# Performance work log

Hardware: AMD Instinct MI355X
Metric: run time of the kernel (lower is better)

## Reference

```python
import jax, jax.numpy as jnp
import numpy as np

N_E = 512; KEY_DIM = 512; E_DIM = 512; E_SPLIT = 8
KT = 0.1; COE_EMA = 0.5; RATE = 1.2
HALF_PI = float(np.pi / 2.0)


def l2n(x, eps=1e-12):
    # torch F.normalize(p=2, dim=-1)
    return x / jnp.maximum(jnp.linalg.norm(x, axis=-1, keepdims=True), eps)


def sphere_emb(feature, t):
    # TimeSphereEncoder: lift unit feature in R^d to R^{d+1} with time angle
    # a = t * (pi/2) / rate ; out = [feature*cos(a), sin(a)]
    a = t * (HALF_PI / RATE)
    return jnp.concatenate([feature * jnp.cos(a)[..., None], jnp.sin(a)[..., None]], axis=-1)


def split_t_f(x):
    # inverse of sphere_emb for unit-norm x: recover (t, sin_component, feature)
    s = x[..., -1]
    t = jnp.arcsin(jnp.clip(s, -1.0, 1.0)) / (HALF_PI / RATE)
    f = l2n(x[..., :-1])
    return t, s, f


def split_norm(v):
    # split_vparams_norm: L2-normalize each of E_SPLIT contiguous chunks
    shp = v.shape
    d = E_DIM // E_SPLIT
    return l2n(v.reshape(shp[:-1] + (E_SPLIT, d))).reshape(shp)


def setup_inputs() -> dict:
    key = jax.random.key(0)
    k = jax.random.split(key, 6)
    key_soft = jax.random.normal(k[0], (32, 1024, KEY_DIM), jnp.float32)
    u_t = jax.random.uniform(k[1], (32, 1024), jnp.float32)
    keys_weight = l2n(jax.random.uniform(k[2], (N_E, KEY_DIM), jnp.float32, -1.0 / N_E, 1.0 / N_E))
    t_keys_weight = (jnp.arange(N_E, dtype=jnp.float32)[:, None]
                     + jax.random.uniform(k[3], (N_E, 1), jnp.float32)) / N_E
    r_keys_weight = jnp.full((N_E, 1), 0.999, jnp.float32)
    vparams_weight = jax.random.uniform(k[4], (N_E, E_DIM), jnp.float32, -1.0 / N_E, 1.0 / N_E)
    return {"key_soft": key_soft, "u_t": u_t, "keys_weight": keys_weight,
            "t_keys_weight": t_keys_weight, "r_keys_weight": r_keys_weight,
            "vparams_weight": vparams_weight}


def _forward(key_soft, u_t, keys_weight, t_keys_weight, r_keys_weight, vparams_weight):
    sg = jax.lax.stop_gradient
    B, T, D = key_soft.shape
    BT = B * T
    # normalize + time-embed tokens
    ks_emb = sphere_emb(l2n(key_soft), u_t)                       # (B,T,D+1)
    ks_flat = ks_emb.reshape(BT, D + 1)
    # codebook keys: normalized, time-embedded, detached, scaled by hardtanh(r)
    keys_norm = sphere_emb(l2n(keys_weight), t_keys_weight[:, 0])  # (n_e,D+1)
    r = jnp.clip(r_keys_weight, 0.0, 1.0)                          # (n_e,1)
    keysA = sg(keys_norm) * r
    score0 = ks_flat @ keysA.T                                     # (BT,n_e)
    idx0 = jnp.argmax(score0, axis=1)
    # --- EMA codebook update (all no-grad) ---
    ks_sg = sg(ks_flat)
    seg = jax.ops.segment_sum(ks_sg, idx0, num_segments=N_E)       # (n_e,D+1)
    cnt = jax.ops.segment_sum(jnp.ones((BT,), ks_sg.dtype), idx0, num_segments=N_E)[:, None]
    mean_ks = jnp.nan_to_num(seg / (1.0 + cnt))
    keys_new_full = l2n(sg(keysA) * COE_EMA + mean_ks * (1.0 - COE_EMA))
    t_new, _, feat_new = split_t_f(keys_new_full)
    index_switch = jnp.argsort(t_new)
    t_sorted = t_new[index_switch]
    keys_feat2 = feat_new[index_switch]
    r2 = jnp.clip(r_keys_weight[index_switch], 0.0, 1.0)
    vparams2 = vparams_weight[index_switch]
    idx1 = index_switch[idx0]
    cnt2 = jax.ops.segment_sum(jnp.ones((BT,), ks_sg.dtype), idx1, num_segments=N_E) + 1.0
    w_cnt = sg(jnp.nan_to_num(1.0 / cnt2)[idx1].reshape(B, T))
    # --- second scoring with updated codebook ---
    keys_norm2 = sphere_emb(l2n(keys_feat2), t_sorted)             # (n_e,D+1)
    keysB = sg(keys_norm2) * r2
    score = ks_flat @ keysB.T                                      # (BT,n_e)
    w = jnp.nan_to_num(jax.nn.softmax(score / KT, axis=-1))
    w_max = jnp.take_along_axis(w, idx1[:, None], axis=-1)[:, 0].reshape(B, T)
    vpn = split_norm(vparams2)
    vp_w = split_norm(w @ sg(vpn))                                 # (BT,e_dim)
    key_w = l2n(w @ sg(keysB))                                     # (BT,D+1)
    vparams_hard = split_norm(vparams2[idx1])
    key_hard_raw = keysB[idx1]
    vparams_hard = vp_w + sg(vparams_hard - vp_w)                  # straight-through
    key_hard = key_w + sg(key_hard_raw - key_w)
    return (idx1.reshape(B, T),
            key_hard.reshape(B, T, D + 1),
            vp_w.reshape(B, T, E_DIM),
            vparams_hard.reshape(B, T, E_DIM),
            w_max, w_cnt, ks_emb)


def reference(key_soft, u_t, keys_weight, t_keys_weight, r_keys_weight, vparams_weight):
    return _forward(key_soft, u_t, keys_weight, t_keys_weight, r_keys_weight, vparams_weight)
```

## Files before the change

kernel.cpp:

```cpp
#include <hip/hip_runtime.h>
#include <math.h>

constexpr int BT  = 32768;
constexpr int D   = 512;
constexpr int D1  = 513;
constexpr int NE  = 512;
constexpr int EDIM = 512;
constexpr int NCH = 128;
constexpr int SUB = 16;
constexpr int P1S = 520;
constexpr int AKP = 544;
#define KA 1.3089969389957472f

typedef _Float16 h16;
typedef _Float16 f16x8 __attribute__((ext_vector_type(8)));
typedef _Float16 f16x4 __attribute__((ext_vector_type(4)));
typedef _Float16 f16x2 __attribute__((ext_vector_type(2)));
typedef float f32x4 __attribute__((ext_vector_type(4)));

__device__ __forceinline__ float wave_sum(float v) {
#pragma unroll
  for (int off = 32; off; off >>= 1) v += __shfl_xor(v, off);
  return v;
}

__global__ __launch_bounds__(256) void k_embed(const float* __restrict__ ks,
                                               const float* __restrict__ ut,
                                               float* __restrict__ emb) {
  int token = blockIdx.x * 4 + (threadIdx.x >> 6);
  int lane = threadIdx.x & 63;
  const float* row = ks + (size_t)token * D;
  float v[8]; float ss = 0.f;
#pragma unroll
  for (int i = 0; i < 8; i++) { v[i] = row[lane + 64 * i]; ss += v[i] * v[i]; }
  ss = wave_sum(ss);
  float inv = 1.0f / fmaxf(sqrtf(ss), 1e-12f);
  float a = ut[token] * KA;
  float c = cosf(a), s = sinf(a);
  float* o = emb + (size_t)token * D1;
#pragma unroll
  for (int i = 0; i < 8; i++) o[lane + 64 * i] = v[i] * inv * c;
  if (lane == 0) o[D] = s;
}

__global__ __launch_bounds__(64) void k_keysA(const float* __restrict__ kw,
                                              const float* __restrict__ tk,
                                              const float* __restrict__ rk,
                                              float* __restrict__ keysA) {
  int e = blockIdx.x; int lane = threadIdx.x;
  const float* row = kw + (size_t)e * D;
  float v[8]; float ss = 0.f;
#pragma unroll
  for (int i = 0; i < 8; i++) { v[i] = row[lane + 64 * i]; ss += v[i] * v[i]; }
  ss = wave_sum(ss);
  float inv = 1.0f / fmaxf(sqrtf(ss), 1e-12f);
  float a = tk[e] * KA;
  float r = fminf(fmaxf(rk[e], 0.f), 1.f);
  float c = cosf(a) * r, s = sinf(a) * r;
  float* o = keysA + (size_t)e * D1;
#pragma unroll
  for (int i = 0; i < 8; i++) o[lane + 64 * i] = v[i] * inv * c;
  if (lane == 0) o[D] = s;
}

__global__ __launch_bounds__(64) void k_split2(const float* __restrict__ in,
                                               h16* __restrict__ out,
                                               int ncol, int kp) {
  int e = blockIdx.x; int lane = threadIdx.x;
  const float* r = in + (size_t)e * ncol;
  h16* o = out + (size_t)e * 2 * kp;
  for (int c = lane; c < kp; c += 64) {
    float x = (c < ncol) ? r[c] * 8.0f : 0.f;
    h16 h = (h16)x;
    o[c] = h;
    o[kp + c] = (h16)(x - (float)h);
  }
}

template <int KP, int EPI, int ASRC>
__global__ __launch_bounds__(256) void k_gemm3(const float* __restrict__ Af,
                                               const h16* __restrict__ Ai,
                                               const h16* __restrict__ Bp,
                                               float* __restrict__ C,
                                               unsigned int* __restrict__ W,
                                               float* __restrict__ pv,
                                               int* __restrict__ pi_,
                                               float* __restrict__ ps) {
  constexpr int NS = KP / 32;
  constexpr int LST = 36;
  __shared__ h16 Ah[128 * LST];
  __shared__ h16 Al[128 * LST];
  __shared__ h16 Bh[128 * LST];
  __shared__ h16 Bl[128 * LST];
  const int tid = threadIdx.x;
  const int bid = blockIdx.x;
  const int wg = (bid & 7) * (gridDim.x >> 3) + (bid >> 3);
  const int m0 = (wg >> 2) * 128;
  const int n0 = (wg & 3) * 128;
  const int nblk = wg & 3;
  const int lane = tid & 63;
  const int wid = tid >> 6;
  const int wr = wid >> 1, wc = wid & 1;
  const int l15 = lane & 15, l4 = lane >> 4;
  const int aB = (wr * 64 + l15) * LST + l4 * 8;
  const int bB = (wc * 64 + l15) * LST + l4 * 8;

  f32x4 acc[4][4] = {};

  auto loadAf = [&](int s, float fv[4][4]) {
    int k0 = s * 32;
    bool guard = (KP == AKP) && (k0 + 32 > D1);
#pragma unroll
    for (int p = 0; p < 4; ++p) {
      int row = (tid >> 3) + 32 * p;
      int fq = tid & 7;
      const float* ap = Af + (size_t)(m0 + row) * D1 + k0 + fq * 4;
      if (!guard) {
#pragma unroll
        for (int j = 0; j < 4; ++j) fv[p][j] = ap[j];
      } else {
#pragma unroll
        for (int j = 0; j < 4; ++j) {
          int c = k0 + fq * 4 + j;
          fv[p][j] = (c < D1) ? ap[j] : 0.f;
        }
      }
    }
  };
  auto writeAf = [&](float fv[4][4]) {
#pragma unroll
    for (int p = 0; p < 4; ++p) {
      int row = (tid >> 3) + 32 * p;
      int fq = tid & 7;
      f16x4 hh, ll;
#pragma unroll
      for (int j = 0; j < 4; ++j) {
        float x = fv[p][j] * 8.0f;
        h16 h = (h16)x;
        hh[j] = h;
        ll[j] = (h16)(x - (float)h);
      }
      *(f16x4*)&Ah[row * LST + fq * 4] = hh;
      *(f16x4*)&Al[row * LST + fq * 4] = ll;
    }
  };
  auto loadAi = [&](int s, uint4 av[4]) {
    int k0 = s * 32;
#pragma unroll
    for (int p = 0; p < 4; ++p) {
      int lin = tid + 256 * p;
      int row = lin >> 3, q = lin & 7;
      av[p] = *(const uint4*)(Ai + (size_t)(m0 + row) * (2 * KP) + k0 * 2 + q * 8);
    }
  };
  auto writeAi = [&](uint4 av[4]) {
#pragma unroll
    for (int p = 0; p < 4; ++p) {
      int lin = tid + 256 * p;
      int row = lin >> 3, q = lin & 7;
      f16x8 r = *(f16x8*)&av[p];
      f16x4 hh = {r[0], r[2], r[4], r[6]};
      f16x4 ll = {r[1], r[3], r[5], r[7]};
      *(f16x4*)&Ah[row * LST + q * 4] = hh;
      *(f16x4*)&Al[row * LST + q * 4] = ll;
    }
  };
  auto loadB = [&](int s, uint4 bv[4]) {
    int k0 = s * 32;
#pragma unroll
    for (int p = 0; p < 4; ++p) {
      int lin = tid + 256 * p;
      int row = (lin >> 2) & 127;
      int half = lin >> 9;
      int q = lin & 3;
      bv[p] = *(const uint4*)(Bp + (size_t)(n0 + row) * (2 * KP) + half * KP + k0 + q * 8);
    }
  };
  auto writeB = [&](uint4 bv[4]) {
#pragma unroll
    for (int p = 0; p < 4; ++p) {
      int lin = tid + 256 * p;
      int row = (lin >> 2) & 127;
      int half = lin >> 9;
      int q = lin & 3;
      h16* dst = half ? Bl : Bh;
      *(uint4*)&dst[row * LST + q * 8] = bv[p];
    }
  };

  {
    uint4 bv[4];
    loadB(0, bv);
    if constexpr (ASRC == 0) { float fv[4][4]; loadAf(0, fv); writeAf(fv); }
    else { uint4 av[4]; loadAi(0, av); writeAi(av); }
    writeB(bv);
  }
  __syncthreads();

  for (int s = 0; s < NS; ++s) {
    uint4 avn[4], bvn[4]; float fvn[4][4];
    if (s + 1 < NS) {
      if constexpr (ASRC == 0) loadAf(s + 1, fvn);
      else loadAi(s + 1, avn);
      loadB(s + 1, bvn);
    }
    f16x8 ah[4], al_[4];
#pragma unroll
    for (int i = 0; i < 4; ++i) {
      ah[i] = *(const f16x8*)&Ah[aB + i * 16 * LST];
      al_[i] = *(const f16x8*)&Al[aB + i * 16 * LST];
    }
#pragma unroll
    for (int j = 0; j < 4; ++j) {
      f16x8 bh_ = *(const f16x8*)&Bh[bB + j * 16 * LST];
      f16x8 bl_ = *(const f16x8*)&Bl[bB + j * 16 * LST];
#pragma unroll
      for (int i = 0; i < 4; ++i) {
        acc[i][j] = __builtin_amdgcn_mfma_f32_16x16x32_f16(ah[i], bh_, acc[i][j], 0, 0, 0);
        acc[i][j] = __builtin_amdgcn_mfma_f32_16x16x32_f16(al_[i], bh_, acc[i][j], 0, 0, 0);
        acc[i][j] = __builtin_amdgcn_mfma_f32_16x16x32_f16(ah[i], bl_, acc[i][j], 0, 0, 0);
      }
    }
    __syncthreads();
    if (s + 1 < NS) {
      if constexpr (ASRC == 0) writeAf(fvn);
      else writeAi(avn);
      writeB(bvn);
    }
    __syncthreads();
  }

  if constexpr (EPI == 1) {
#pragma unroll
    for (int i = 0; i < 4; ++i)
#pragma unroll
      for (int r = 0; r < 4; ++r) {
        float ss = 0.f;
#pragma unroll
        for (int j = 0; j < 4; ++j) ss += acc[i][j][r] * acc[i][j][r];
        ss += __shfl_xor(ss, 1); ss += __shfl_xor(ss, 2);
        ss += __shfl_xor(ss, 4); ss += __shfl_xor(ss, 8);
        float inv = 1.0f / fmaxf(sqrtf(ss), 1e-12f);
        int row = m0 + wr * 64 + i * 16 + l4 * 4 + r;
        float* cp = C + (size_t)row * 512 + n0 + wc * 64 + l15;
#pragma unroll
        for (int j = 0; j < 4; ++j) cp[j * 16] = acc[i][j][r] * inv;
      }
  } else if constexpr (EPI == 2) {
    float* lv = (float*)Ah;
    int*   li = (int*)Bh;
#pragma unroll
    for (int i = 0; i < 4; ++i)
#pragma unroll
      for (int r = 0; r < 4; ++r) {
        float bv = -INFINITY; int bidx = 0x7fffffff;
#pragma unroll
        for (int j = 0; j < 4; ++j) {
          float val = acc[i][j][r] * 0.015625f;
          int col = n0 + wc * 64 + j * 16 + l15;
          if (val > bv || (val == bv && col < bidx)) { bv = val; bidx = col; }
        }
#pragma unroll
        for (int off = 1; off < 16; off <<= 1) {
          float ov = __shfl_xor(bv, off);
          int oi = __shfl_xor(bidx, off);
          if (ov > bv || (ov == bv && oi < bidx)) { bv = ov; bidx = oi; }
        }
        if (l15 == 0) {
          int lr = wr * 64 + i * 16 + l4 * 4 + r;
          lv[wc * 128 + lr] = bv; li[wc * 128 + lr] = bidx;
        }
      }
    __syncthreads();
    if (tid < 128) {
      float v0 = lv[tid], v1 = lv[128 + tid];
      int i0 = li[tid], i1 = li[128 + tid];
      bool sec = (v1 > v0) || (v1 == v0 && i1 < i0);
      int row = m0 + tid;
      pv[(size_t)row * 4 + nblk] = sec ? v1 : v0;
      pi_[(size_t)row * 4 + nblk] = sec ? i1 : i0;
    }
  } else if constexpr (EPI == 3) {
    float* psW = (float*)Bh;
#pragma unroll
    for (int i = 0; i < 4; ++i)
#pragma unroll
      for (int r = 0; r < 4; ++r) {
        int row = m0 + wr * 64 + i * 16 + l4 * 4 + r;
        unsigned int* wp = W + (size_t)row * 512 + n0 + wc * 64 + l15;
        float se = 0.f;
#pragma unroll
        for (int j = 0; j < 4; ++j) {
          float v = acc[i][j][r] * 0.015625f;
          float w = __expf(10.f * v);
          se += w;
          h16 hh = (h16)w;
          f16x2 pk = {hh, (h16)(w - (float)hh)};
          wp[j * 16] = *(unsigned int*)&pk;
        }
        se += __shfl_xor(se, 1); se += __shfl_xor(se, 2);
        se += __shfl_xor(se, 4); se += __shfl_xor(se, 8);
        if (l15 == 0) psW[wc * 128 + wr * 64 + i * 16 + l4 * 4 + r] = se;
      }
    __syncthreads();
    if (tid < 128)
      ps[(size_t)(m0 + tid) * 4 + nblk] = psW[tid] + psW[128 + tid];
  }
}

__global__ __launch_bounds__(256) void k_argmax_fin(const float* __restrict__ pval,
                                                    const int* __restrict__ pidx,
                                                    int* __restrict__ idx0) {
  int t = blockIdx.x * 256 + threadIdx.x;
  float bv = pval[(size_t)t * 4];
  int bi = pidx[(size_t)t * 4];
#pragma unroll
  for (int b = 1; b < 4; ++b) {
    float v = pval[(size_t)t * 4 + b];
    if (v > bv) { bv = v; bi = pidx[(size_t)t * 4 + b]; }
  }
  idx0[t] = bi;
}

__global__ __launch_bounds__(256) void k_smfin(const float* __restrict__ ps,
                                               const unsigned int* __restrict__ W,
                                               const int* __restrict__ idx1,
                                               float* __restrict__ O4) {
  int t = blockIdx.x * 256 + threadIdx.x;
  float S = ps[(size_t)t * 4] + ps[(size_t)t * 4 + 1]
          + ps[(size_t)t * 4 + 2] + ps[(size_t)t * 4 + 3];
  unsigned int u = W[(size_t)t * 512 + idx1[t]];
  f16x2 pk = *(f16x2*)&u;
  float wsel = (float)pk[0] + (float)pk[1];
  O4[t] = wsel / S;
}

__global__ __launch_bounds__(256) void k_hist_chunks(const int* __restrict__ idx0,
                                                     int* __restrict__ hist2,
                                                     int* __restrict__ myrank) {
  __shared__ int lidx[256];
  __shared__ int hist[NE];
  int tid = threadIdx.x;
  int chunk = blockIdx.x;
  int t = chunk * 256 + tid;
  lidx[tid] = idx0[t];
  hist[tid] = 0; hist[tid + 256] = 0;
  __syncthreads();
  int j = lidx[tid];
  int rank = 0;
  for (int i = 0; i < tid; ++i) rank += (lidx[i] == j);
  myrank[t] = rank;
  atomicAdd(&hist[j], 1);
  __syncthreads();
  hist2[chunk * NE + tid] = hist[tid];
  hist2[chunk * NE + tid + 256] = hist[tid + 256];
}

__global__ __launch_bounds__(512) void k_scan(const int* __restrict__ hist2,
                                              int* __restrict__ offs,
                                              int* __restrict__ chunk_base,
                                              float* __restrict__ cntf) {
  __shared__ int sh[NE];
  int c = threadIdx.x;
  int tot = 0;
  for (int k = 0; k < NCH; ++k) tot += hist2[k * NE + c];
  cntf[c] = (float)tot;
  sh[c] = tot;
  __syncthreads();
  for (int off = 1; off < NE; off <<= 1) {
    int v = (c >= off) ? sh[c - off] : 0;
    __syncthreads();
    sh[c] += v;
    __syncthreads();
  }
  int excl = sh[c] - tot;
  offs[c] = excl;
  int run = excl;
  for (int k = 0; k < NCH; ++k) {
    chunk_base[k * NE + c] = run;
    run += hist2[k * NE + c];
  }
}

__global__ __launch_bounds__(256) void k_scatter(const int* __restrict__ idx0,
                                                 const int* __restrict__ myrank,
                                                 const int* __restrict__ chunk_base,
                                                 int* __restrict__ tok_sorted) {
  int tid = threadIdx.x;
  int chunk = blockIdx.x;
  int t = chunk * 256 + tid;
  int j = idx0[t];
  tok_sorted[chunk_base[chunk * NE + j] + myrank[t]] = t;
}

__global__ __launch_bounds__(256) void k_seg1(const int* __restrict__ tok_sorted,
                                              const int* __restrict__ offs,
                                              const float* __restrict__ cntf,
                                              const float* __restrict__ emb,
                                              float* __restrict__ part1) {
  __shared__ float part[4][512];
  __shared__ float p512[4];
  int e = blockIdx.x, sub = blockIdx.y;
  int tid = threadIdx.x;
  int wave = tid >> 6, lane = tid & 63;
  int start = offs[e];
  int n = (int)cntf[e];
  float acc[8] = {}; float a512 = 0.f;
  for (int k = sub * 4 + wave; k < n; k += SUB * 4) {
    int t = tok_sorted[start + k];
    const float* row = emb + (size_t)t * D1;
#pragma unroll
    for (int i = 0; i < 8; ++i) acc[i] += row[lane + 64 * i];
    if (lane == 0) a512 += row[512];
  }
#pragma unroll
  for (int i = 0; i < 8; ++i) part[wave][lane + 64 * i] = acc[i];
  if (lane == 0) p512[wave] = a512;
  __syncthreads();
  float* o = part1 + (size_t)(e * SUB + sub) * P1S;
  o[tid] = part[0][tid] + part[1][tid] + part[2][tid] + part[3][tid];
  o[tid + 256] = part[0][tid + 256] + part[1][tid + 256] + part[2][tid + 256] + part[3][tid + 256];
  if (tid == 0) o[512] = p512[0] + p512[1] + p512[2] + p512[3];
}

__global__ __launch_bounds__(256) void k_seg2(const float* __restrict__ part1,
                                              const float* __restrict__ cntf,
                                              const float* __restrict__ keysA,
                                              float* __restrict__ feat,
                                              float* __restrict__ tnew) {
  __shared__ float r4[4];
  __shared__ float r4b[4];
  int e = blockIdx.x;
  int tid = threadIdx.x;
  int wave = tid >> 6, lane = tid & 63;
  float s0 = 0.f, s1 = 0.f, s512 = 0.f;
  for (int sub = 0; sub < SUB; ++sub) {
    const float* p = part1 + (size_t)(e * SUB + sub) * P1S;
    s0 += p[tid]; s1 += p[tid + 256]; s512 += p[512];
  }
  float c = cntf[e];
  float rinv = 1.0f / (1.0f + c);
  float x0 = keysA[(size_t)e * D1 + tid] * 0.5f + (s0 * rinv) * 0.5f;
  float x1 = keysA[(size_t)e * D1 + tid + 256] * 0.5f + (s1 * rinv) * 0.5f;
  float x512 = keysA[(size_t)e * D1 + 512] * 0.5f + (s512 * rinv) * 0.5f;
  float ssp = x0 * x0 + x1 * x1;
  float w = wave_sum(ssp);
  if (lane == 0) r4[wave] = w;
  __syncthreads();
  float ss = r4[0] + r4[1] + r4[2] + r4[3] + x512 * x512;
  float inv = 1.0f / fmaxf(sqrtf(ss), 1e-12f);
  if (tid == 0) {
    float sc = fminf(fmaxf(x512 * inv, -1.0f), 1.0f);
    tnew[e] = asinf(sc) / KA;
  }
  float f0 = x0 * inv, f1 = x1 * inv;
  float ssp2 = f0 * f0 + f1 * f1;
  float w2 = wave_sum(ssp2);
  if (lane == 0) r4b[wave] = w2;
  __syncthreads();
  float ss2 = r4b[0] + r4b[1] + r4b[2] + r4b[3];
  float inv2 = 1.0f / fmaxf(sqrtf(ss2), 1e-12f);
  feat[(size_t)e * D + tid] = f0 * inv2;
  feat[(size_t)e * D + tid + 256] = f1 * inv2;
}

__global__ __launch_bounds__(512) void k_argsort(const float* __restrict__ tnew,
                                                 int* __restrict__ perm) {
  __shared__ float t[NE];
  int i = threadIdx.x;
  t[i] = tnew[i];
  __syncthreads();
  float ti = t[i];
  int rank = 0;
  for (int j = 0; j < NE; j++) {
    float tj = t[j];
    rank += (tj < ti) || (tj == ti && j < i);
  }
  perm[rank] = i;
}

__global__ __launch_bounds__(64) void k_build(const int* __restrict__ perm,
                                              const float* __restrict__ tnew,
                                              const float* __restrict__ rk,
                                              const float* __restrict__ feat,
                                              const float* __restrict__ vparams,
                                              float* __restrict__ keysB,
                                              float* __restrict__ vpn,
                                              h16* __restrict__ BV) {
  int p = blockIdx.x; int lane = threadIdx.x;
  int src = perm[p];
  float t = tnew[src];
  float a = t * KA;
  float r2 = fminf(fmaxf(rk[src], 0.f), 1.f);
  float f[8]; float ss = 0.f;
#pragma unroll
  for (int i = 0; i < 8; i++) { f[i] = feat[(size_t)src * D + lane + 64 * i]; ss += f[i] * f[i]; }
  ss = wave_sum(ss);
  float inv = 1.0f / fmaxf(sqrtf(ss), 1e-12f);
  float c = cosf(a) * r2, s = sinf(a) * r2;
#pragma unroll
  for (int i = 0; i < 8; i++) keysB[(size_t)p * D1 + lane + 64 * i] = f[i] * inv * c;
  if (lane == 0) keysB[(size_t)p * D1 + D] = s;
#pragma unroll
  for (int i = 0; i < 8; i++) {
    float vp = vparams[(size_t)src * EDIM + lane + 64 * i];
    float ssc = wave_sum(vp * vp);
    float invc = 1.0f / fmaxf(sqrtf(ssc), 1e-12f);
    float val = vp * invc;
    int d = lane + 64 * i;
    vpn[(size_t)p * EDIM + d] = val;
    float x = val * 8.0f;
    h16 hi = (h16)x;
    BV[(size_t)d * (2 * NE) + p] = hi;
    BV[(size_t)d * (2 * NE) + NE + p] = (h16)(x - (float)hi);
  }
}

__global__ __launch_bounds__(256) void k_idx1(const int* __restrict__ idx0,
                                              const int* __restrict__ perm,
                                              int* __restrict__ idx1,
                                              float* __restrict__ O0) {
  int t = blockIdx.x * 256 + threadIdx.x;
  int j = perm[idx0[t]];
  idx1[t] = j;
  O0[t] = (float)j;
}

__global__ __launch_bounds__(256) void k_gather(const int* __restrict__ idx1,
                                                const int* __restrict__ perm,
                                                const float* __restrict__ cntf,
                                                const float* __restrict__ keysB,
                                                const float* __restrict__ vpn,
                                                float* __restrict__ O1,
                                                float* __restrict__ O3,
                                                float* __restrict__ O5) {
  int t = blockIdx.x * 4 + (threadIdx.x >> 6);
  int lane = threadIdx.x & 63;
  int j = idx1[t];
#pragma unroll
  for (int i = 0; i < 9; i++) {
    int d = lane + 64 * i;
    if (d < D1) O1[(size_t)t * D1 + d] = keysB[(size_t)j * D1 + d];
  }
#pragma unroll
  for (int i = 0; i < 8; i++) {
    int d = lane + 64 * i;
    O3[(size_t)t * EDIM + d] = vpn[(size_t)j * EDIM + d];
  }
  if (lane == 0) O5[t] = 1.0f / (cntf[perm[j]] + 1.0f);
}

extern "C" void kernel_launch(void* const* d_in, const int* in_sizes, int n_in,
                              void* d_out, int out_size, void* d_ws, size_t ws_size,
                              hipStream_t stream) {
  const float* key_soft = (const float*)d_in[0];
  const float* u_t      = (const float*)d_in[1];
  const float* keys_w   = (const float*)d_in[2];
  const float* t_keys   = (const float*)d_in[3];
  const float* r_keys   = (const float*)d_in[4];
  const float* vparams  = (const float*)d_in[5];

  float* out = (float*)d_out;
  float* O0 = out;
  float* O1 = O0 + (size_t)BT;
  float* O2 = O1 + (size_t)BT * D1;
  float* O3 = O2 + (size_t)BT * EDIM;
  float* O4 = O3 + (size_t)BT * EDIM;
  float* O5 = O4 + (size_t)BT;
  float* O6 = O5 + (size_t)BT;

  float* ws = (float*)d_ws;
  size_t off = 0;
  auto alloc = [&](size_t n) { float* p = ws + off; off += (n + 63) & ~(size_t)63; return p; };
  unsigned int* w16 = (unsigned int*)alloc((size_t)BT * 512);
  float* part1  = alloc((size_t)NE * SUB * P1S);
  float* keysA  = alloc((size_t)NE * D1);
  float* keysB  = alloc((size_t)NE * D1);
  float* feat   = alloc((size_t)NE * D);
  float* vpn    = alloc((size_t)NE * EDIM);
  float* tnew   = alloc(NE);
  float* cntf   = alloc(NE);
  h16*   BA     = (h16*)alloc((size_t)NE * AKP);
  h16*   BB     = (h16*)alloc((size_t)NE * AKP);
  h16*   BV     = (h16*)alloc((size_t)EDIM * NE);
  float* pval   = alloc((size_t)BT * 4);
  int*   pidx   = (int*)alloc((size_t)BT * 4);
  float* ps2    = alloc((size_t)BT * 4);
  int*   idx0   = (int*)alloc(BT);
  int*   idx1   = (int*)alloc(BT);
  int*   perm   = (int*)alloc(NE);
  int*   myrank = (int*)alloc(BT);
  int*   tok_sorted = (int*)alloc(BT);
  int*   hist2  = (int*)alloc((size_t)NCH * NE);
  int*   chunk_base = (int*)alloc((size_t)NCH * NE);
  int*   offsb  = (int*)alloc(NE);

  k_embed<<<BT / 4, 256, 0, stream>>>(key_soft, u_t, O6);
  k_keysA<<<NE, 64, 0, stream>>>(keys_w, t_keys, r_keys, keysA);
  k_split2<<<NE, 64, 0, stream>>>(keysA, BA, D1, AKP);
  k_gemm3<AKP, 2, 0><<<1024, 256, 0, stream>>>(O6, nullptr, BA,
                                               nullptr, nullptr, pval, pidx, nullptr);
  k_argmax_fin<<<BT / 256, 256, 0, stream>>>(pval, pidx, idx0);
  k_hist_chunks<<<NCH, 256, 0, stream>>>(idx0, hist2, myrank);
  k_scan<<<1, NE, 0, stream>>>(hist2, offsb, chunk_base, cntf);
  k_scatter<<<NCH, 256, 0, stream>>>(idx0, myrank, chunk_base, tok_sorted);
  k_seg1<<<dim3(NE, SUB), 256, 0, stream>>>(tok_sorted, offsb, cntf, O6, part1);
  k_seg2<<<NE, 256, 0, stream>>>(part1, cntf, keysA, feat, tnew);
  k_argsort<<<1, NE, 0, stream>>>(tnew, perm);
  k_build<<<NE, 64, 0, stream>>>(perm, tnew, r_keys, feat, vparams, keysB, vpn, BV);
  k_split2<<<NE, 64, 0, stream>>>(keysB, BB, D1, AKP);
  k_idx1<<<BT / 256, 256, 0, stream>>>(idx0, perm, idx1, O0);
  k_gemm3<AKP, 3, 0><<<1024, 256, 0, stream>>>(O6, nullptr, BB,
                                               nullptr, w16, nullptr, nullptr, ps2);
  k_smfin<<<BT / 256, 256, 0, stream>>>(ps2, w16, idx1, O4);
  k_gemm3<512, 1, 1><<<1024, 256, 0, stream>>>(nullptr, (const h16*)w16, BV,
                                               O2, nullptr, nullptr, nullptr, nullptr);
  k_gather<<<BT / 4, 256, 0, stream>>>(idx1, perm, cntf, keysB, vpn, O1, O3, O5);
}
```

Before: 505.4 us.

## Cut split-fp16 GEMM terms per stage and store softmax weights as single fp16

Adds a TERMS template parameter so each GEMM runs only as many split-precision MFMA products as it needs. The first scoring GEMM keeps three terms because argmax needs accuracy. The second scoring GEMM drops the B-low term, and the weighted-value GEMM uses a single fp16 term. The softmax weight buffer shrinks from packed hi/lo fp16 pairs to one fp16 per element, halving its write and read traffic. The embed kernel is also changed to vectorized float4 loads. The price is lower precision in w and vp_w, which risks tolerance failures.

```diff
diff --git a/kernel.cpp b/kernel.cpp
--- a/kernel.cpp
+++ b/kernel.cpp
@@ -15,7 +15,6 @@
 typedef _Float16 h16;
 typedef _Float16 f16x8 __attribute__((ext_vector_type(8)));
 typedef _Float16 f16x4 __attribute__((ext_vector_type(4)));
-typedef _Float16 f16x2 __attribute__((ext_vector_type(2)));
 typedef float f32x4 __attribute__((ext_vector_type(4)));
 
 __device__ __forceinline__ float wave_sum(float v) {
@@ -29,18 +28,20 @@
                                                float* __restrict__ emb) {
   int token = blockIdx.x * 4 + (threadIdx.x >> 6);
   int lane = threadIdx.x & 63;
-  const float* row = ks + (size_t)token * D;
-  float v[8]; float ss = 0.f;
-#pragma unroll
-  for (int i = 0; i < 8; i++) { v[i] = row[lane + 64 * i]; ss += v[i] * v[i]; }
+  const float4* row4 = (const float4*)(ks + (size_t)token * D);
+  float4 va = row4[lane * 2];
+  float4 vb = row4[lane * 2 + 1];
+  float ss = va.x * va.x + va.y * va.y + va.z * va.z + va.w * va.w
+           + vb.x * vb.x + vb.y * vb.y + vb.z * vb.z + vb.w * vb.w;
   ss = wave_sum(ss);
   float inv = 1.0f / fmaxf(sqrtf(ss), 1e-12f);
   float a = ut[token] * KA;
   float c = cosf(a), s = sinf(a);
-  float* o = emb + (size_t)token * D1;
-#pragma unroll
-  for (int i = 0; i < 8; i++) o[lane + 64 * i] = v[i] * inv * c;
-  if (lane == 0) o[D] = s;
+  float ic = inv * c;
+  float* o = emb + (size_t)token * D1 + lane * 8;
+  o[0] = va.x * ic; o[1] = va.y * ic; o[2] = va.z * ic; o[3] = va.w * ic;
+  o[4] = vb.x * ic; o[5] = vb.y * ic; o[6] = vb.z * ic; o[7] = vb.w * ic;
+  if (lane == 0) emb[(size_t)token * D1 + D] = s;
 }
 
 __global__ __launch_bounds__(64) void k_keysA(const float* __restrict__ kw,
@@ -77,21 +78,21 @@
   }
 }
 
-template <int KP, int EPI, int ASRC>
+template <int KP, int EPI, int ASRC, int TERMS>
 __global__ __launch_bounds__(256) void k_gemm3(const float* __restrict__ Af,
                                                const h16* __restrict__ Ai,
                                                const h16* __restrict__ Bp,
                                                float* __restrict__ C,
-                                               unsigned int* __restrict__ W,
+                                               unsigned short* __restrict__ W,
                                                float* __restrict__ pv,
                                                int* __restrict__ pi_,
                                                float* __restrict__ ps) {
   constexpr int NS = KP / 32;
   constexpr int LST = 36;
   __shared__ h16 Ah[128 * LST];
-  __shared__ h16 Al[128 * LST];
+  __shared__ h16 Al[(TERMS >= 2) ? 128 * LST : 1];
   __shared__ h16 Bh[128 * LST];
-  __shared__ h16 Bl[128 * LST];
+  __shared__ h16 Bl[(TERMS >= 3) ? 128 * LST : 1];
   const int tid = threadIdx.x;
   const int bid = blockIdx.x;
   const int wg = (bid & 7) * (gridDim.x >> 3) + (bid >> 3);
@@ -141,34 +142,31 @@
         ll[j] = (h16)(x - (float)h);
       }
       *(f16x4*)&Ah[row * LST + fq * 4] = hh;
-      *(f16x4*)&Al[row * LST + fq * 4] = ll;
+      if constexpr (TERMS >= 2) *(f16x4*)&Al[row * LST + fq * 4] = ll;
     }
   };
-  auto loadAi = [&](int s, uint4 av[4]) {
+  auto loadAi = [&](int s, uint4 av[2]) {
     int k0 = s * 32;
 #pragma unroll
-    for (int p = 0; p < 4; ++p) {
+    for (int p = 0; p < 2; ++p) {
       int lin = tid + 256 * p;
-      int row = lin >> 3, q = lin & 7;
-      av[p] = *(const uint4*)(Ai + (size_t)(m0 + row) * (2 * KP) + k0 * 2 + q * 8);
+      int row = lin >> 2, q = lin & 3;
+      av[p] = *(const uint4*)(Ai + (size_t)(m0 + row) * 512 + k0 + q * 8);
     }
   };
-  auto writeAi = [&](uint4 av[4]) {
-#pragma unroll
-    for (int p = 0; p < 4; ++p) {
+  auto writeAi = [&](uint4 av[2]) {
+#pragma unroll
+    for (int p = 0; p < 2; ++p) {
       int lin = tid + 256 * p;
-      int row = lin >> 3, q = lin & 7;
-      f16x8 r = *(f16x8*)&av[p];
-      f16x4 hh = {r[0], r[2], r[4], r[6]};
-      f16x4 ll = {r[1], r[3], r[5], r[7]};
-      *(f16x4*)&Ah[row * LST + q * 4] = hh;
-      *(f16x4*)&Al[row * LST + q * 4] = ll;
+      int row = lin >> 2, q = lin & 3;
+      *(uint4*)&Ah[row * LST + q * 8] = av[p];
     }
   };
-  auto loadB = [&](int s, uint4 bv[4]) {
+  constexpr int BPASS = (TERMS >= 3) ? 4 : 2;
+  auto loadB = [&](int s, uint4 bv[BPASS]) {
     int k0 = s * 32;
 #pragma unroll
-    for (int p = 0; p < 4; ++p) {
+    for (int p = 0; p < BPASS; ++p) {
       int lin = tid + 256 * p;
       int row = (lin >> 2) & 127;
       int half = lin >> 9;
@@ -176,29 +174,29 @@
       bv[p] = *(const uint4*)(Bp + (size_t)(n0 + row) * (2 * KP) + half * KP + k0 + q * 8);
     }
   };
-  auto writeB = [&](uint4 bv[4]) {
-#pragma unroll
-    for (int p = 0; p < 4; ++p) {
+  auto writeB = [&](uint4 bv[BPASS]) {
+#pragma unroll
+    for (int p = 0; p < BPASS; ++p) {
       int lin = tid + 256 * p;
       int row = (lin >> 2) & 127;
       int half = lin >> 9;
       int q = lin & 3;
-      h16* dst = half ? Bl : Bh;
+      h16* dst = (half && TERMS >= 3) ? Bl : Bh;
       *(uint4*)&dst[row * LST + q * 8] = bv[p];
     }
   };
 
   {
-    uint4 bv[4];
+    uint4 bv[BPASS];
     loadB(0, bv);
     if constexpr (ASRC == 0) { float fv[4][4]; loadAf(0, fv); writeAf(fv); }
-    else { uint4 av[4]; loadAi(0, av); writeAi(av); }
+    else { uint4 av[2]; loadAi(0, av); writeAi(av); }
     writeB(bv);
   }
   __syncthreads();
 
   for (int s = 0; s < NS; ++s) {
-    uint4 avn[4], bvn[4]; float fvn[4][4];
+    uint4 avn[2], bvn[BPASS]; float fvn[4][4];
     if (s + 1 < NS) {
       if constexpr (ASRC == 0) loadAf(s + 1, fvn);
       else loadAi(s + 1, avn);
@@ -208,17 +206,20 @@
 #pragma unroll
     for (int i = 0; i < 4; ++i) {
       ah[i] = *(const f16x8*)&Ah[aB + i * 16 * LST];
-      al_[i] = *(const f16x8*)&Al[aB + i * 16 * LST];
+      if constexpr (TERMS >= 2) al_[i] = *(const f16x8*)&Al[aB + i * 16 * LST];
     }
 #pragma unroll
     for (int j = 0; j < 4; ++j) {
       f16x8 bh_ = *(const f16x8*)&Bh[bB + j * 16 * LST];
-      f16x8 bl_ = *(const f16x8*)&Bl[bB + j * 16 * LST];
+      f16x8 bl_;
+      if constexpr (TERMS >= 3) bl_ = *(const f16x8*)&Bl[bB + j * 16 * LST];
 #pragma unroll
       for (int i = 0; i < 4; ++i) {
         acc[i][j] = __builtin_amdgcn_mfma_f32_16x16x32_f16(ah[i], bh_, acc[i][j], 0, 0, 0);
-        acc[i][j] = __builtin_amdgcn_mfma_f32_16x16x32_f16(al_[i], bh_, acc[i][j], 0, 0, 0);
-        acc[i][j] = __builtin_amdgcn_mfma_f32_16x16x32_f16(ah[i], bl_, acc[i][j], 0, 0, 0);
+        if constexpr (TERMS >= 2)
+          acc[i][j] = __builtin_amdgcn_mfma_f32_16x16x32_f16(al_[i], bh_, acc[i][j], 0, 0, 0);
+        if constexpr (TERMS >= 3)
+          acc[i][j] = __builtin_amdgcn_mfma_f32_16x16x32_f16(ah[i], bl_, acc[i][j], 0, 0, 0);
       }
     }
     __syncthreads();
@@ -287,7 +288,7 @@
 #pragma unroll
       for (int r = 0; r < 4; ++r) {
         int row = m0 + wr * 64 + i * 16 + l4 * 4 + r;
-        unsigned int* wp = W + (size_t)row * 512 + n0 + wc * 64 + l15;
+        unsigned short* wp = W + (size_t)row * 512 + n0 + wc * 64 + l15;
         float se = 0.f;
 #pragma unroll
         for (int j = 0; j < 4; ++j) {
@@ -295,8 +296,7 @@
           float w = __expf(10.f * v);
           se += w;
           h16 hh = (h16)w;
-          f16x2 pk = {hh, (h16)(w - (float)hh)};
-          wp[j * 16] = *(unsigned int*)&pk;
+          wp[j * 16] = *(unsigned short*)&hh;
         }
         se += __shfl_xor(se, 1); se += __shfl_xor(se, 2);
         se += __shfl_xor(se, 4); se += __shfl_xor(se, 8);
@@ -323,15 +323,14 @@
 }
 
 __global__ __launch_bounds__(256) void k_smfin(const float* __restrict__ ps,
-                                               const unsigned int* __restrict__ W,
+                                               const unsigned short* __restrict__ W,
                                                const int* __restrict__ idx1,
                                                float* __restrict__ O4) {
   int t = blockIdx.x * 256 + threadIdx.x;
   float S = ps[(size_t)t * 4] + ps[(size_t)t * 4 + 1]
           + ps[(size_t)t * 4 + 2] + ps[(size_t)t * 4 + 3];
-  unsigned int u = W[(size_t)t * 512 + idx1[t]];
-  f16x2 pk = *(f16x2*)&u;
-  float wsel = (float)pk[0] + (float)pk[1];
+  unsigned short u = W[(size_t)t * 512 + idx1[t]];
+  float wsel = (float)(*(const h16*)&u);
   O4[t] = wsel / S;
 }
 
@@ -572,7 +571,7 @@
   float* ws = (float*)d_ws;
   size_t off = 0;
   auto alloc = [&](size_t n) { float* p = ws + off; off += (n + 63) & ~(size_t)63; return p; };
-  unsigned int* w16 = (unsigned int*)alloc((size_t)BT * 512);
+  unsigned short* w16 = (unsigned short*)alloc((size_t)BT * 256);
   float* part1  = alloc((size_t)NE * SUB * P1S);
   float* keysA  = alloc((size_t)NE * D1);
   float* keysB  = alloc((size_t)NE * D1);
@@ -598,8 +597,8 @@
   k_embed<<<BT / 4, 256, 0, stream>>>(key_soft, u_t, O6);
   k_keysA<<<NE, 64, 0, stream>>>(keys_w, t_keys, r_keys, keysA);
   k_split2<<<NE, 64, 0, stream>>>(keysA, BA, D1, AKP);
-  k_gemm3<AKP, 2, 0><<<1024, 256, 0, stream>>>(O6, nullptr, BA,
-                                               nullptr, nullptr, pval, pidx, nullptr);
+  k_gemm3<AKP, 2, 0, 3><<<1024, 256, 0, stream>>>(O6, nullptr, BA,
+                                                  nullptr, nullptr, pval, pidx, nullptr);
   k_argmax_fin<<<BT / 256, 256, 0, stream>>>(pval, pidx, idx0);
   k_hist_chunks<<<NCH, 256, 0, stream>>>(idx0, hist2, myrank);
   k_scan<<<1, NE, 0, stream>>>(hist2, offsb, chunk_base, cntf);
@@ -610,10 +609,10 @@
   k_build<<<NE, 64, 0, stream>>>(perm, tnew, r_keys, feat, vparams, keysB, vpn, BV);
   k_split2<<<NE, 64, 0, stream>>>(keysB, BB, D1, AKP);
   k_idx1<<<BT / 256, 256, 0, stream>>>(idx0, perm, idx1, O0);
-  k_gemm3<AKP, 3, 0><<<1024, 256, 0, stream>>>(O6, nullptr, BB,
-                                               nullptr, w16, nullptr, nullptr, ps2);
+  k_gemm3<AKP, 3, 0, 2><<<1024, 256, 0, stream>>>(O6, nullptr, BB,
+                                                  nullptr, w16, nullptr, nullptr, ps2);
   k_smfin<<<BT / 256, 256, 0, stream>>>(ps2, w16, idx1, O4);
-  k_gemm3<512, 1, 1><<<1024, 256, 0, stream>>>(nullptr, (const h16*)w16, BV,
-                                               O2, nullptr, nullptr, nullptr, nullptr);
+  k_gemm3<512, 1, 2, 1><<<1024, 256, 0, stream>>>(nullptr, (const h16*)w16, BV,
+                                                  O2, nullptr, nullptr, nullptr, nullptr);
   k_gather<<<BT / 4, 256, 0, stream>>>(idx1, perm, cntf, keysB, vpn, O1, O3, O5);
 }
```

New measurement: 443.8 us. 12.2% less time.
